# Kernel optimization log

Measured on AMD Instinct MI355X. Metric: run time of the kernel, lower is better.

Reference implementation:

```python
import jax, jax.numpy as jnp
import numpy as np

INPUT_DIM = 64
DIM = 256
N_EMB = 2048
M_BOOK = 4
MASK_RATIO = 0.1
N = 32768


def _bn(h, g, b):
    # BatchNorm1d in training mode: batch statistics (biased variance)
    mu = h.mean(axis=0)
    var = ((h - mu) ** 2).mean(axis=0)
    return (h - mu) * jax.lax.rsqrt(var + 1e-5) * g + b


def _quantize(r, E):
    # squared-distance via dot expansion: ||r||^2 - 2 r.E^T + ||E||^2  -> [N, K]
    d = (r * r).sum(axis=1, keepdims=True) - 2.0 * (r @ E.T) + (E * E).sum(axis=1)
    idx = jnp.argmin(d, axis=1)
    return E[idx]


def setup_inputs() -> dict:
    key = jax.random.key(0)
    ks = jax.random.split(key, 24)
    s = 0.02
    cb_lim = 1.0 / N_EMB
    inp = {
        "x": jax.random.normal(ks[0], (N, INPUT_DIM), jnp.float32),
        "pos": jax.random.uniform(ks[1], (1, INPUT_DIM), jnp.float32, -cb_lim, cb_lim),
        # encoder: Linear(64,128), BN128, Linear(128,256), BN256, Linear(256,256)
        "e_w0": jax.random.normal(ks[2], (INPUT_DIM, 128), jnp.float32) * s,
        "e_b0": jnp.zeros((128,), jnp.float32),
        "e_g0": jnp.ones((128,), jnp.float32),
        "e_bt0": jnp.zeros((128,), jnp.float32),
        "e_w1": jax.random.normal(ks[3], (128, 256), jnp.float32) * s,
        "e_b1": jnp.zeros((256,), jnp.float32),
        "e_g1": jnp.ones((256,), jnp.float32),
        "e_bt1": jnp.zeros((256,), jnp.float32),
        "e_w2": jax.random.normal(ks[4], (256, DIM), jnp.float32) * s,
        "e_b2": jnp.zeros((DIM,), jnp.float32),
        # codebooks: [M, K, C], uniform(-1/K, 1/K)
        "codebooks": jax.random.uniform(ks[5], (M_BOOK, N_EMB, DIM), jnp.float32, -cb_lim, cb_lim),
        # decoder: Linear(256,256), BN256, Linear(256,128), BN128, Linear(128,64)
        "d_w0": jax.random.normal(ks[6], (DIM, 256), jnp.float32) * s,
        "d_b0": jnp.zeros((256,), jnp.float32),
        "d_g0": jnp.ones((256,), jnp.float32),
        "d_bt0": jnp.zeros((256,), jnp.float32),
        "d_w1": jax.random.normal(ks[7], (256, 128), jnp.float32) * s,
        "d_b1": jnp.zeros((128,), jnp.float32),
        "d_g1": jnp.ones((128,), jnp.float32),
        "d_bt1": jnp.zeros((128,), jnp.float32),
        "d_w2": jax.random.normal(ks[8], (128, INPUT_DIM), jnp.float32) * s,
        "d_b2": jnp.zeros((INPUT_DIM,), jnp.float32),
    }
    return inp


def reference(x, pos, e_w0, e_b0, e_g0, e_bt0, e_w1, e_b1, e_g1, e_bt1, e_w2, e_b2,
              codebooks, d_w0, d_b0, d_g0, d_bt0, d_w1, d_b1, d_g1, d_bt1, d_w2, d_b2):
    # mask = x[0,:].bernoulli_(mask_ratio): in-place overwrites row 0 with 0/1 samples
    bern = jax.random.bernoulli(jax.random.key(42), MASK_RATIO, (x.shape[1],)).astype(x.dtype)
    x = x.at[0].set(bern)
    x = jnp.where(bern.astype(bool)[None, :], 0.0, x)
    x = x + pos

    # encoder (Dropout treated as identity / eval; BN uses batch stats as in training)
    h = jax.nn.relu(_bn(x @ e_w0 + e_b0, e_g0, e_bt0))
    h = jax.nn.relu(_bn(h @ e_w1 + e_b1, e_g1, e_bt1))
    ze = h @ e_w2 + e_b2  # [N, C]

    res_list, ce_list = [], []
    res = ze
    for m in range(M_BOOK):
        if m > 0:
            res = res_list[m - 1] - ce_list[m - 1]
        ce = _quantize(res, codebooks[m])
        res_list.append(res)
        ce_list.append(ce)

    zq = sum(ce_list)
    decoder_input = ze + jax.lax.stop_gradient(zq - ze)  # straight-through

    h = jax.nn.relu(_bn(decoder_input @ d_w0 + d_b0, d_g0, d_bt0))
    h = jax.nn.relu(_bn(h @ d_w1 + d_b1, d_g1, d_bt1))
    x_hat = h @ d_w2 + d_b2
    return x_hat, jnp.stack(res_list, 0), jnp.stack(ce_list, 0)
```

## Files before the change

kernel.cpp:

```cpp
#include <hip/hip_runtime.h>

#define N_ROWS 32768

typedef unsigned short u16;
typedef __attribute__((ext_vector_type(8))) short short8;
typedef __attribute__((ext_vector_type(4))) float f32x4;
typedef __attribute__((ext_vector_type(4))) u16 us4;

__device__ __forceinline__ unsigned rotl32(unsigned x, unsigned r) {
  return (x << r) | (x >> (32u - r));
}
__device__ __forceinline__ void tf_round(unsigned &x0, unsigned &x1, unsigned r) {
  x0 += x1; x1 = rotl32(x1, r); x1 ^= x0;
}

__global__ void mask_kernel(float* __restrict__ mask) {
  int j = threadIdx.x;
  if (j >= 64) return;
  const unsigned k0 = 0u, k1 = 42u;
  const unsigned k2 = 0x1BD11BDAu ^ k0 ^ k1;
  unsigned x0 = 0u;
  unsigned x1 = (unsigned)j;
  x0 += k0; x1 += k1;
  tf_round(x0, x1, 13); tf_round(x0, x1, 15); tf_round(x0, x1, 26); tf_round(x0, x1, 6);
  x0 += k1; x1 += k2 + 1u;
  tf_round(x0, x1, 17); tf_round(x0, x1, 29); tf_round(x0, x1, 16); tf_round(x0, x1, 24);
  x0 += k2; x1 += k0 + 2u;
  tf_round(x0, x1, 13); tf_round(x0, x1, 15); tf_round(x0, x1, 26); tf_round(x0, x1, 6);
  x0 += k0; x1 += k1 + 3u;
  tf_round(x0, x1, 17); tf_round(x0, x1, 29); tf_round(x0, x1, 16); tf_round(x0, x1, 24);
  x0 += k1; x1 += k2 + 4u;
  tf_round(x0, x1, 13); tf_round(x0, x1, 15); tf_round(x0, x1, 26); tf_round(x0, x1, 6);
  x0 += k2; x1 += k0 + 5u;
  unsigned bits = x0 ^ x1;
  float u = __uint_as_float((bits >> 9) | 0x3f800000u) - 1.0f;
  mask[j] = (u < 0.1f) ? 1.0f : 0.0f;
}

__global__ void norme_kernel(const float* __restrict__ cb, float* __restrict__ nE) {
#pragma clang fp contract(off)
  int k = blockIdx.x * blockDim.x + threadIdx.x;
  const float* r = cb + (size_t)k * 256;
  float halves[2];
#pragma unroll
  for (int h = 0; h < 2; h++) {
    float a[8];
#pragma unroll
    for (int j = 0; j < 8; j++) a[j] = 0.0f;
    for (int t = 0; t < 16; t++) {
      float4 v0 = *(const float4*)&r[h * 128 + 8 * t];
      float4 v1 = *(const float4*)&r[h * 128 + 8 * t + 4];
      a[0] = a[0] + v0.x * v0.x; a[1] = a[1] + v0.y * v0.y;
      a[2] = a[2] + v0.z * v0.z; a[3] = a[3] + v0.w * v0.w;
      a[4] = a[4] + v1.x * v1.x; a[5] = a[5] + v1.y * v1.y;
      a[6] = a[6] + v1.z * v1.z; a[7] = a[7] + v1.w * v1.w;
    }
    halves[h] = ((a[0] + a[1]) + (a[2] + a[3])) + ((a[4] + a[5]) + (a[6] + a[7]));
  }
  nE[k] = halves[0] + halves[1];
}

__global__ void rownorm_kernel(const float* __restrict__ R, float* __restrict__ rr) {
#pragma clang fp contract(off)
  int tid = threadIdx.x;
  int row = blockIdx.x * 64 + (tid >> 2);
  int q = tid & 3;
  int h = q >> 1;
  int j0 = (q & 1) << 2;
  const float* p = R + (size_t)row * 256 + h * 128 + j0;
  float a[4] = {0.f, 0.f, 0.f, 0.f};
  for (int t = 0; t < 16; t++) {
    float4 v = *(const float4*)&p[8 * t];
    a[0] = a[0] + v.x * v.x; a[1] = a[1] + v.y * v.y;
    a[2] = a[2] + v.z * v.z; a[3] = a[3] + v.w * v.w;
  }
  float s = (a[0] + a[1]) + (a[2] + a[3]);
  float half = s + __shfl_xor(s, 1, 4);
  float tot = half + __shfl_xor(half, 2, 4);
  if (q == 0) rr[row] = tot;
}

__device__ __forceinline__ u16 f2bf(float x) {
  unsigned u = __float_as_uint(x);
  unsigned r = u + 0x7fffu + ((u >> 16) & 1u);
  return (u16)(r >> 16);
}
__device__ __forceinline__ float bf2f(u16 h) {
  return __uint_as_float(((unsigned)h) << 16);
}

__global__ void cvt_kernel(const float* __restrict__ in, u16* __restrict__ out) {
  int gid = blockIdx.x * 256 + threadIdx.x;
  int row = gid >> 5, seg = gid & 31;
  const float* p = in + (size_t)row * 256 + seg * 8;
  u16* H = out + (size_t)row * 512 + seg * 8;
  float4 a = *(const float4*)p;
  float4 b = *(const float4*)(p + 4);
  float v[8] = {a.x, a.y, a.z, a.w, b.x, b.y, b.z, b.w};
  u16 hh[8], ll[8];
#pragma unroll
  for (int t = 0; t < 8; t++) {
    hh[t] = f2bf(v[t]);
    ll[t] = f2bf(v[t] - bf2f(hh[t]));
  }
  us4 H0 = {hh[0], hh[1], hh[2], hh[3]};
  us4 H1 = {hh[4], hh[5], hh[6], hh[7]};
  us4 L0 = {ll[0], ll[1], ll[2], ll[3]};
  us4 L1 = {ll[4], ll[5], ll[6], ll[7]};
  *(us4*)&H[0] = H0;  *(us4*)&H[4] = H1;
  *(us4*)&H[256] = L0; *(us4*)&H[260] = L1;
}

__global__ void bnprep_kernel(const double* __restrict__ psum, const double* __restrict__ psq,
                              const float* __restrict__ g, const float* __restrict__ bt,
                              float* __restrict__ a, float* __restrict__ c, int F) {
  int f = blockIdx.x * blockDim.x + threadIdx.x;
  if (f >= F) return;
  double s = 0.0, q = 0.0;
  const double* ps = psum + (size_t)f * 512;
  const double* pq = psq + (size_t)f * 512;
  for (int b = 0; b < 512; b++) { s += ps[b]; q += pq[b]; }
  double mu  = s * (1.0 / 32768.0);
  double var = q * (1.0 / 32768.0) - mu * mu;
  double inv = (double)g[f] / sqrt(var + 1e-5);
  a[f] = (float)inv;
  c[f] = (float)((double)bt[f] - mu * inv);
}

template <int MODE, int STATS>
__global__ __launch_bounds__(256)
void gemm64(const float* __restrict__ A, const float* __restrict__ W,
            const float* __restrict__ bias, const float* __restrict__ p0,
            const float* __restrict__ p1, const float* __restrict__ A3,
            float* __restrict__ out,
            double* __restrict__ psum, double* __restrict__ psq, int K, int F) {
  __shared__ float As[16][68];
  __shared__ float Bs[16][68];
  __shared__ double psumS[4][64];
  __shared__ double psqS[4][64];
  const int tid = threadIdx.x;
  const int row0 = blockIdx.y << 6;
  const int col0 = blockIdx.x << 6;
  const int ty = tid >> 4, tx = tid & 15;
  const int ar = tid >> 2, aq = (tid & 3) << 2;
  const int bk = tid >> 4, bc = (tid & 15) << 2;
  float acc[4][4] = {};
  for (int k0 = 0; k0 < K; k0 += 16) {
    const size_t aoff = (size_t)(row0 + ar) * K + k0 + aq;
    float4 av = *(const float4*)&A[aoff];
    float4 bv = *(const float4*)&W[(size_t)(k0 + bk) * F + col0 + bc];
    float a4[4] = { av.x, av.y, av.z, av.w };
    if (MODE == 0) {
#pragma unroll
      for (int j = 0; j < 4; j++) {
        int gk = k0 + aq + j;
        float m = p0[gk];
        float v = (m != 0.0f || (row0 + ar) == 0) ? 0.0f : a4[j];
        a4[j] = v + p1[gk];
      }
    } else if (MODE == 1) {
#pragma unroll
      for (int j = 0; j < 4; j++) {
        int gk = k0 + aq + j;
        a4[j] = fmaxf(fmaf(a4[j], p0[gk], p1[gk]), 0.0f);
      }
    } else if (MODE == 3) {
      float4 v1 = *(const float4*)&p0[aoff];
      float4 v2 = *(const float4*)&p1[aoff];
      float4 v3 = *(const float4*)&A3[aoff];
      a4[0] = ((a4[0] + v1.x) + v2.x) + v3.x;
      a4[1] = ((a4[1] + v1.y) + v2.y) + v3.y;
      a4[2] = ((a4[2] + v1.z) + v2.z) + v3.z;
      a4[3] = ((a4[3] + v1.w) + v2.w) + v3.w;
    }
    __syncthreads();
#pragma unroll
    for (int j = 0; j < 4; j++) As[aq + j][ar] = a4[j];
    *(float4*)&Bs[bk][bc] = bv;
    __syncthreads();
#pragma unroll
    for (int kc = 0; kc < 16; kc++) {
      float4 a = *(const float4*)&As[kc][ty << 2];
      float4 b = *(const float4*)&Bs[kc][tx << 2];
      float a_[4] = { a.x, a.y, a.z, a.w };
      float b_[4] = { b.x, b.y, b.z, b.w };
#pragma unroll
      for (int i = 0; i < 4; i++)
#pragma unroll
        for (int j = 0; j < 4; j++)
          acc[i][j] = fmaf(a_[i], b_[j], acc[i][j]);
    }
  }
  float bj[4];
#pragma unroll
  for (int j = 0; j < 4; j++) bj[j] = bias[col0 + (tx << 2) + j];
  double sj[4] = {}, qj[4] = {};
#pragma unroll
  for (int i = 0; i < 4; i++) {
    float v[4];
#pragma unroll
    for (int j = 0; j < 4; j++) {
      v[j] = acc[i][j] + bj[j];
      if (STATS) {
        sj[j] += (double)v[j];
        qj[j] += (double)v[j] * (double)v[j];
      }
    }
    float4 vv = { v[0], v[1], v[2], v[3] };
    *(float4*)&out[(size_t)(row0 + (ty << 2) + i) * F + col0 + (tx << 2)] = vv;
  }
  if (STATS) {
#pragma unroll
    for (int j = 0; j < 4; j++) {
      sj[j] += __shfl_down(sj[j], 32);
      sj[j] += __shfl_down(sj[j], 16);
      qj[j] += __shfl_down(qj[j], 32);
      qj[j] += __shfl_down(qj[j], 16);
    }
    const int w = tid >> 6;
    if ((tid & 63) < 16) {
#pragma unroll
      for (int j = 0; j < 4; j++) {
        psumS[w][((tid & 15) << 2) + j] = sj[j];
        psqS[w][((tid & 15) << 2) + j] = qj[j];
      }
    }
    __syncthreads();
    if (tid < 64) {
      double ds = (psumS[0][tid] + psumS[1][tid]) + (psumS[2][tid] + psumS[3][tid]);
      double dq = (psqS[0][tid] + psqS[1][tid]) + (psqS[2][tid] + psqS[3][tid]);
      psum[(size_t)(col0 + tid) * 512 + blockIdx.y] = ds;
      psq[(size_t)(col0 + tid) * 512 + blockIdx.y] = dq;
    }
  }
}

__device__ __forceinline__ void gld16(const void* gp, void* lp) {
  __builtin_amdgcn_global_load_lds(
      (__attribute__((address_space(1))) unsigned int*)gp,
      (__attribute__((address_space(3))) unsigned int*)lp,
      16, 0, 0);
}

#define MFMA16(a, b, c) __builtin_amdgcn_mfma_f32_16x16x32_bf16(a, b, c, 0, 0, 0)

__global__ __launch_bounds__(256, 2)
void quantize_mfma(const float* __restrict__ Rf, u16* Rcvt,
                   const float* __restrict__ Ef, const u16* __restrict__ Ecvt,
                   const float* __restrict__ nEp, const float* __restrict__ rr,
                   float* __restrict__ ce, float* __restrict__ resn) {
  __shared__ __align__(16) u16 As[2][64][32];
  __shared__ __align__(16) u16 Bs[2][128][32];
  __shared__ float sD1[2][64], sD2[2][64];
  __shared__ int sI1[2][64], sI2[2][64];
  __shared__ int s_iA[64], s_iB[64];

  const int tid = threadIdx.x;
  const int row0 = blockIdx.x << 6;
  const int w = tid >> 6;
  const int lane = tid & 63;
  const int wr = w >> 1, wc = w & 1;
  const int l15 = lane & 15, l4 = lane >> 4;

  float rrv[8];
#pragma unroll
  for (int s = 0; s < 8; s++)
    rrv[s] = rr[row0 + 32 * wr + 16 * (s >> 2) + 4 * l4 + (s & 3)];

  float bd1[8], bd2[8];
  int bi1[8], bi2[8];
#pragma unroll
  for (int s = 0; s < 8; s++) { bd1[s] = 3.0e38f; bd2[s] = 3.0e38f; bi1[s] = 0; bi2[s] = 1; }

  const int str = lane >> 2;
  const int sdst = (lane & 3) << 3;
  const int ssrc = (((lane & 3) ^ ((lane >> 3) & 3)) << 3);
  const int krd = ((l15 >> 1) & 3) << 3;

  for (int n0 = 0; n0 < 2048; n0 += 128) {
    f32x4 acc[2][4] = {};
    for (int k0 = 0; k0 < 256; k0 += 32) {
      __syncthreads();
      {
        const u16* gA = Rcvt + (size_t)(row0 + 16 * w + str) * 512 + k0 + ssrc;
        gld16(gA,       &As[0][16 * w + str][sdst]);
        gld16(gA + 256, &As[1][16 * w + str][sdst]);
#pragma unroll
        for (int q = 0; q < 2; q++) {
          const int rb = 32 * w + 16 * q + str;
          const u16* gB = Ecvt + (size_t)(n0 + rb) * 512 + k0 + ssrc;
          gld16(gB,       &Bs[0][rb][sdst]);
          gld16(gB + 256, &Bs[1][rb][sdst]);
        }
      }
      __syncthreads();
      short8 ah[2], al[2], bh[4], bl[4];
#pragma unroll
      for (int i = 0; i < 2; i++) {
        const int ro = 32 * wr + 16 * i + l15;
        ah[i] = *(const short8*)&As[0][ro][(l4 << 3) ^ krd];
        al[i] = *(const short8*)&As[1][ro][(l4 << 3) ^ krd];
      }
#pragma unroll
      for (int j = 0; j < 4; j++) {
        const int ro = 64 * wc + 16 * j + l15;
        bh[j] = *(const short8*)&Bs[0][ro][(l4 << 3) ^ krd];
        bl[j] = *(const short8*)&Bs[1][ro][(l4 << 3) ^ krd];
      }
#pragma unroll
      for (int i = 0; i < 2; i++)
#pragma unroll
        for (int j = 0; j < 4; j++) {
          acc[i][j] = MFMA16(ah[i], bh[j], acc[i][j]);
          acc[i][j] = MFMA16(ah[i], bl[j], acc[i][j]);
          acc[i][j] = MFMA16(al[i], bh[j], acc[i][j]);
        }
    }
#pragma unroll
    for (int j = 0; j < 4; j++) {
      const int col = n0 + 64 * wc + 16 * j + l15;
      const float nn = nEp[col];
#pragma unroll
      for (int i = 0; i < 2; i++)
#pragma unroll
        for (int r = 0; r < 4; r++) {
          const int s = i * 4 + r;
          float t = rrv[s] - 2.0f * acc[i][j][r];
          float d = t + nn;
          if (d < bd2[s]) {
            if (d < bd1[s]) {
              bd2[s] = bd1[s]; bi2[s] = bi1[s];
              bd1[s] = d; bi1[s] = col;
            } else {
              bd2[s] = d; bi2[s] = col;
            }
          }
        }
    }
  }

#pragma unroll
  for (int s = 0; s < 8; s++) {
    float d1 = bd1[s], d2 = bd2[s];
    int i1 = bi1[s], i2 = bi2[s];
#pragma unroll
    for (int off = 1; off <= 8; off <<= 1) {
      float e1 = __shfl_xor(d1, off, 16);
      float e2 = __shfl_xor(d2, off, 16);
      int j1 = __shfl_xor(i1, off, 16);
      int j2 = __shfl_xor(i2, off, 16);
      if (e1 < d1 || (e1 == d1 && j1 < i1)) {
        bool ps = (d1 < e2) || (d1 == e2 && i1 < j2);
        d2 = ps ? d1 : e2; i2 = ps ? i1 : j2;
        d1 = e1; i1 = j1;
      } else {
        bool ps = (e1 < d2) || (e1 == d2 && j1 < i2);
        if (ps) { d2 = e1; i2 = j1; }
      }
    }
    if (l15 == 0) {
      int lr = 32 * wr + 16 * (s >> 2) + 4 * l4 + (s & 3);
      sD1[wc][lr] = d1; sI1[wc][lr] = i1;
      sD2[wc][lr] = d2; sI2[wc][lr] = i2;
    }
  }
  __syncthreads();
  if (tid < 64) {
    float d1 = sD1[0][tid], d2 = sD2[0][tid];
    int i1 = sI1[0][tid], i2 = sI2[0][tid];
    float e1 = sD1[1][tid], e2 = sD2[1][tid];
    int j1 = sI1[1][tid], j2 = sI2[1][tid];
    int iA, iB;
    if (e1 < d1 || (e1 == d1 && j1 < i1)) {
      iA = j1;
      bool ps = (d1 < e2) || (d1 == e2 && i1 < j2);
      iB = ps ? i1 : j2;
    } else {
      iA = i1;
      bool ps = (e1 < d2) || (e1 == d2 && j1 < i2);
      iB = ps ? j1 : i2;
    }
    s_iA[tid] = iA; s_iB[tid] = iB;
  }
  __syncthreads();

  const int orow = tid >> 2;
  const int q = tid & 3;
  const int gr = row0 + orow;
  const int iA = s_iA[orow], iB = s_iB[orow];
  const float* __restrict__ Rr = Rf + (size_t)gr * 256;
  const float* __restrict__ EA = Ef + (size_t)iA * 256;
  const float* __restrict__ EB = Ef + (size_t)iB * 256;
  float pa[4] = {0.f, 0.f, 0.f, 0.f}, pb[4] = {0.f, 0.f, 0.f, 0.f};
  const int c0 = q << 6;
  for (int t = 0; t < 16; t++) {
    float4 rv = *(const float4*)&Rr[c0 + 4 * t];
    float4 ea = *(const float4*)&EA[c0 + 4 * t];
    float4 eb = *(const float4*)&EB[c0 + 4 * t];
    pa[0] = fmaf(rv.x, ea.x, pa[0]); pa[1] = fmaf(rv.y, ea.y, pa[1]);
    pa[2] = fmaf(rv.z, ea.z, pa[2]); pa[3] = fmaf(rv.w, ea.w, pa[3]);
    pb[0] = fmaf(rv.x, eb.x, pb[0]); pb[1] = fmaf(rv.y, eb.y, pb[1]);
    pb[2] = fmaf(rv.z, eb.z, pb[2]); pb[3] = fmaf(rv.w, eb.w, pb[3]);
  }
  float sA = (pa[0] + pa[1]) + (pa[2] + pa[3]);
  float sB = (pb[0] + pb[1]) + (pb[2] + pb[3]);
  sA += __shfl_xor(sA, 1, 4); sA += __shfl_xor(sA, 2, 4);
  sB += __shfl_xor(sB, 1, 4); sB += __shfl_xor(sB, 2, 4);
  const float rrow = rr[gr];
  float dA = (rrow - 2.0f * sA) + nEp[iA];
  float dB = (rrow - 2.0f * sB) + nEp[iB];
  const int idx = (dB < dA || (dB == dA && iB < iA)) ? iB : iA;

  const int oc0 = q << 6;
  const float* __restrict__ Er = Ef + (size_t)idx * 256;
  float* __restrict__ Cr = ce + (size_t)gr * 256;
  if (resn) {
    float* __restrict__ Nr = resn + (size_t)gr * 256;
    u16* Hr = Rcvt + (size_t)gr * 512;
    for (int c = oc0; c < oc0 + 64; c += 4) {
      float4 e = *(const float4*)&Er[c];
      float4 r = *(const float4*)&Rr[c];
      *(float4*)&Cr[c] = e;
      float4 dd = { r.x - e.x, r.y - e.y, r.z - e.z, r.w - e.w };
      *(float4*)&Nr[c] = dd;
      u16 h0 = f2bf(dd.x), h1 = f2bf(dd.y), h2 = f2bf(dd.z), h3 = f2bf(dd.w);
      us4 hv = { h0, h1, h2, h3 };
      us4 lv = { f2bf(dd.x - bf2f(h0)), f2bf(dd.y - bf2f(h1)),
                 f2bf(dd.z - bf2f(h2)), f2bf(dd.w - bf2f(h3)) };
      *(us4*)&Hr[c] = hv;
      *(us4*)&Hr[256 + c] = lv;
    }
  } else {
    for (int c = oc0; c < oc0 + 64; c += 4) {
      float4 e = *(const float4*)&Er[c];
      *(float4*)&Cr[c] = e;
    }
  }
}

extern "C" void kernel_launch(void* const* d_in, const int* in_sizes, int n_in,
                              void* d_out, int out_size, void* d_ws, size_t ws_size,
                              hipStream_t stream) {
  (void)in_sizes; (void)n_in; (void)out_size; (void)ws_size;
  const float* x     = (const float*)d_in[0];
  const float* pos   = (const float*)d_in[1];
  const float* e_w0  = (const float*)d_in[2];
  const float* e_b0  = (const float*)d_in[3];
  const float* e_g0  = (const float*)d_in[4];
  const float* e_bt0 = (const float*)d_in[5];
  const float* e_w1  = (const float*)d_in[6];
  const float* e_b1  = (const float*)d_in[7];
  const float* e_g1  = (const float*)d_in[8];
  const float* e_bt1 = (const float*)d_in[9];
  const float* e_w2  = (const float*)d_in[10];
  const float* e_b2  = (const float*)d_in[11];
  const float* cb    = (const float*)d_in[12];
  const float* d_w0  = (const float*)d_in[13];
  const float* d_b0  = (const float*)d_in[14];
  const float* d_g0  = (const float*)d_in[15];
  const float* d_bt0 = (const float*)d_in[16];
  const float* d_w1  = (const float*)d_in[17];
  const float* d_b1  = (const float*)d_in[18];
  const float* d_g1  = (const float*)d_in[19];
  const float* d_bt1 = (const float*)d_in[20];
  const float* d_w2  = (const float*)d_in[21];
  const float* d_b2  = (const float*)d_in[22];

  float* ws = (float*)d_ws;
  float* mask   = ws + 64;
  float* aff    = ws + 128;
  float* nE     = ws + 1664;
  double* psum  = (double*)(ws + 16384);
  double* psq   = (double*)(ws + 278528);
  float* g1     = ws + 540672;
  float* g0     = g1 + (size_t)N_ROWS * 256;
  float* rr     = g0 + (size_t)N_ROWS * 128;

  float* e0a = aff + 0;    float* e0c = aff + 128;
  float* e1a = aff + 256;  float* e1c = aff + 512;
  float* d0a = aff + 768;  float* d0c = aff + 1024;
  float* d1a = aff + 1280; float* d1c = aff + 1408;

  float* outp = (float*)d_out;
  float* xhat = outp;
  float* res0 = outp + (size_t)N_ROWS * 64;
  float* res1 = res0 + (size_t)N_ROWS * 256;
  float* res2 = res1 + (size_t)N_ROWS * 256;
  float* res3 = res2 + (size_t)N_ROWS * 256;
  float* ce0  = res0 + (size_t)4 * N_ROWS * 256;
  float* ce1  = ce0 + (size_t)N_ROWS * 256;
  float* ce2  = ce1 + (size_t)N_ROWS * 256;
  float* ce3  = ce2 + (size_t)N_ROWS * 256;

  float* h0 = ce2;
  float* h1 = ce3;
  u16* Ecvt = (u16*)xhat;
  u16* Rcvt = (u16*)ce3;

  mask_kernel<<<1, 64, 0, stream>>>(mask);
  norme_kernel<<<32, 256, 0, stream>>>(cb, nE);
  cvt_kernel<<<1024, 256, 0, stream>>>(cb, Ecvt);

  gemm64<0, 1><<<dim3(2, 512), 256, 0, stream>>>(x, e_w0, e_b0, mask, pos, nullptr,
                                                 h0, psum, psq, 64, 128);
  bnprep_kernel<<<1, 256, 0, stream>>>(psum, psq, e_g0, e_bt0, e0a, e0c, 128);
  gemm64<1, 1><<<dim3(4, 512), 256, 0, stream>>>(h0, e_w1, e_b1, e0a, e0c, nullptr,
                                                 h1, psum, psq, 128, 256);
  bnprep_kernel<<<1, 256, 0, stream>>>(psum, psq, e_g1, e_bt1, e1a, e1c, 256);
  gemm64<1, 0><<<dim3(4, 512), 256, 0, stream>>>(h1, e_w2, e_b2, e1a, e1c, nullptr,
                                                 res0, nullptr, nullptr, 256, 256);

  cvt_kernel<<<4096, 256, 0, stream>>>(res0, Rcvt);
  rownorm_kernel<<<512, 256, 0, stream>>>(res0, rr);
  quantize_mfma<<<512, 256, 0, stream>>>(res0, Rcvt,
                                         cb + (size_t)0 * 2048 * 256,
                                         Ecvt + (size_t)0 * 2048 * 512,
                                         nE + 0, rr, ce0, res1);
  rownorm_kernel<<<512, 256, 0, stream>>>(res1, rr);
  quantize_mfma<<<512, 256, 0, stream>>>(res1, Rcvt,
                                         cb + (size_t)1 * 2048 * 256,
                                         Ecvt + (size_t)1 * 2048 * 512,
                                         nE + 2048, rr, ce1, res2);
  rownorm_kernel<<<512, 256, 0, stream>>>(res2, rr);
  quantize_mfma<<<512, 256, 0, stream>>>(res2, Rcvt,
                                         cb + (size_t)2 * 2048 * 256,
                                         Ecvt + (size_t)2 * 2048 * 512,
                                         nE + 4096, rr, ce2, res3);
  rownorm_kernel<<<512, 256, 0, stream>>>(res3, rr);
  quantize_mfma<<<512, 256, 0, stream>>>(res3, Rcvt,
                                         cb + (size_t)3 * 2048 * 256,
                                         Ecvt + (size_t)3 * 2048 * 512,
                                         nE + 6144, rr, ce3, nullptr);

  gemm64<3, 1><<<dim3(4, 512), 256, 0, stream>>>(ce0, d_w0, d_b0, ce1, ce2, ce3,
                                                 g1, psum, psq, 256, 256);
  bnprep_kernel<<<1, 256, 0, stream>>>(psum, psq, d_g0, d_bt0, d0a, d0c, 256);
  gemm64<1, 1><<<dim3(2, 512), 256, 0, stream>>>(g1, d_w1, d_b1, d0a, d0c, nullptr,
                                                 g0, psum, psq, 256, 128);
  bnprep_kernel<<<1, 256, 0, stream>>>(psum, psq, d_g1, d_bt1, d1a, d1c, 128);
  gemm64<1, 0><<<dim3(1, 512), 256, 0, stream>>>(g0, d_w2, d_b2, d1a, d1c, nullptr,
                                                 xhat, nullptr, nullptr, 128, 64);
}
```

Before: 1.703 ms.

## Double-buffer LDS tiles in quantize kernel to overlap loads with MFMA

Flattens the nested codebook/K loops into a single 128-step loop and double-buffers the A and B LDS tiles. The next tile's global-to-LDS load is issued before computing on the current one, and only one barrier is needed per step. The codebook norm loads are also hoisted to the start of each column block. This doubles LDS use per block, which may limit occupancy at 2 blocks per CU, and the single barrier per step relies on the async LDS load being complete by the time that barrier is reached.

```diff
diff --git a/kernel.cpp b/kernel.cpp
--- a/kernel.cpp
+++ b/kernel.cpp
@@ -249,8 +249,8 @@
                    const float* __restrict__ Ef, const u16* __restrict__ Ecvt,
                    const float* __restrict__ nEp, const float* __restrict__ rr,
                    float* __restrict__ ce, float* __restrict__ resn) {
-  __shared__ __align__(16) u16 As[2][64][32];
-  __shared__ __align__(16) u16 Bs[2][128][32];
+  __shared__ __align__(16) u16 As[2][2][64][32];
+  __shared__ __align__(16) u16 Bs[2][2][128][32];
   __shared__ float sD1[2][64], sD2[2][64];
   __shared__ int sI1[2][64], sI2[2][64];
   __shared__ int s_iA[64], s_iB[64];
@@ -277,67 +277,93 @@
   const int ssrc = (((lane & 3) ^ ((lane >> 3) & 3)) << 3);
   const int krd = ((l15 >> 1) & 3) << 3;
 
-  for (int n0 = 0; n0 < 2048; n0 += 128) {
-    f32x4 acc[2][4] = {};
-    for (int k0 = 0; k0 < 256; k0 += 32) {
-      __syncthreads();
-      {
-        const u16* gA = Rcvt + (size_t)(row0 + 16 * w + str) * 512 + k0 + ssrc;
-        gld16(gA,       &As[0][16 * w + str][sdst]);
-        gld16(gA + 256, &As[1][16 * w + str][sdst]);
-#pragma unroll
-        for (int q = 0; q < 2; q++) {
-          const int rb = 32 * w + 16 * q + str;
-          const u16* gB = Ecvt + (size_t)(n0 + rb) * 512 + k0 + ssrc;
-          gld16(gB,       &Bs[0][rb][sdst]);
-          gld16(gB + 256, &Bs[1][rb][sdst]);
-        }
-      }
-      __syncthreads();
-      short8 ah[2], al[2], bh[4], bl[4];
-#pragma unroll
-      for (int i = 0; i < 2; i++) {
-        const int ro = 32 * wr + 16 * i + l15;
-        ah[i] = *(const short8*)&As[0][ro][(l4 << 3) ^ krd];
-        al[i] = *(const short8*)&As[1][ro][(l4 << 3) ^ krd];
-      }
+  const u16* gAbase = Rcvt + (size_t)(row0 + 16 * w + str) * 512 + ssrc;
+  const u16* gB0 = Ecvt + (size_t)(32 * w + str) * 512 + ssrc;
+  const u16* gB1 = Ecvt + (size_t)(32 * w + 16 + str) * 512 + ssrc;
+  const int rb0 = 32 * w + str, rb1 = 32 * w + 16 + str;
+
+#define STAGE(b, t)                                                         \
+  {                                                                         \
+    const int n0_ = ((t) >> 3) << 7, k0_ = ((t) & 7) << 5;                  \
+    const u16* gA_ = gAbase + k0_;                                          \
+    gld16(gA_,       &As[b][0][16 * w + str][sdst]);                        \
+    gld16(gA_ + 256, &As[b][1][16 * w + str][sdst]);                        \
+    const u16* g0_ = gB0 + (size_t)n0_ * 512 + k0_;                         \
+    const u16* g1_ = gB1 + (size_t)n0_ * 512 + k0_;                         \
+    gld16(g0_,       &Bs[b][0][rb0][sdst]);                                 \
+    gld16(g0_ + 256, &Bs[b][1][rb0][sdst]);                                 \
+    gld16(g1_,       &Bs[b][0][rb1][sdst]);                                 \
+    gld16(g1_ + 256, &Bs[b][1][rb1][sdst]);                                 \
+  }
+
+  STAGE(0, 0);
+  __syncthreads();
+
+  f32x4 acc[2][4] = {};
+  float nn4[4];
+#pragma unroll 2
+  for (int t = 0; t < 128; t++) {
+    const int b = t & 1;
+    if ((t & 7) == 0) {
+      const int n0 = (t >> 3) << 7;
+#pragma unroll
+      for (int j = 0; j < 4; j++) nn4[j] = nEp[n0 + 64 * wc + 16 * j + l15];
+    }
+    if (t + 1 < 128) STAGE(b ^ 1, t + 1);
+
+    short8 ah[2], al[2], bh[4], bl[4];
+#pragma unroll
+    for (int i = 0; i < 2; i++) {
+      const int ro = 32 * wr + 16 * i + l15;
+      ah[i] = *(const short8*)&As[b][0][ro][(l4 << 3) ^ krd];
+      al[i] = *(const short8*)&As[b][1][ro][(l4 << 3) ^ krd];
+    }
+#pragma unroll
+    for (int j = 0; j < 4; j++) {
+      const int ro = 64 * wc + 16 * j + l15;
+      bh[j] = *(const short8*)&Bs[b][0][ro][(l4 << 3) ^ krd];
+      bl[j] = *(const short8*)&Bs[b][1][ro][(l4 << 3) ^ krd];
+    }
+#pragma unroll
+    for (int i = 0; i < 2; i++)
 #pragma unroll
       for (int j = 0; j < 4; j++) {
-        const int ro = 64 * wc + 16 * j + l15;
-        bh[j] = *(const short8*)&Bs[0][ro][(l4 << 3) ^ krd];
-        bl[j] = *(const short8*)&Bs[1][ro][(l4 << 3) ^ krd];
-      }
-#pragma unroll
-      for (int i = 0; i < 2; i++)
-#pragma unroll
-        for (int j = 0; j < 4; j++) {
-          acc[i][j] = MFMA16(ah[i], bh[j], acc[i][j]);
-          acc[i][j] = MFMA16(ah[i], bl[j], acc[i][j]);
-          acc[i][j] = MFMA16(al[i], bh[j], acc[i][j]);
-        }
-    }
-#pragma unroll
-    for (int j = 0; j < 4; j++) {
-      const int col = n0 + 64 * wc + 16 * j + l15;
-      const float nn = nEp[col];
-#pragma unroll
-      for (int i = 0; i < 2; i++)
-#pragma unroll
-        for (int r = 0; r < 4; r++) {
-          const int s = i * 4 + r;
-          float t = rrv[s] - 2.0f * acc[i][j][r];
-          float d = t + nn;
-          if (d < bd2[s]) {
-            if (d < bd1[s]) {
-              bd2[s] = bd1[s]; bi2[s] = bi1[s];
-              bd1[s] = d; bi1[s] = col;
-            } else {
-              bd2[s] = d; bi2[s] = col;
+        acc[i][j] = MFMA16(ah[i], bh[j], acc[i][j]);
+        acc[i][j] = MFMA16(ah[i], bl[j], acc[i][j]);
+        acc[i][j] = MFMA16(al[i], bh[j], acc[i][j]);
+      }
+
+    if ((t & 7) == 7) {
+      const int n0 = (t >> 3) << 7;
+#pragma unroll
+      for (int j = 0; j < 4; j++) {
+        const int col = n0 + 64 * wc + 16 * j + l15;
+        const float nn = nn4[j];
+#pragma unroll
+        for (int i = 0; i < 2; i++)
+#pragma unroll
+          for (int r = 0; r < 4; r++) {
+            const int s = i * 4 + r;
+            float tt = rrv[s] - 2.0f * acc[i][j][r];
+            float d = tt + nn;
+            if (d < bd2[s]) {
+              if (d < bd1[s]) {
+                bd2[s] = bd1[s]; bi2[s] = bi1[s];
+                bd1[s] = d; bi1[s] = col;
+              } else {
+                bd2[s] = d; bi2[s] = col;
+              }
             }
           }
-        }
-    }
-  }
+      }
+#pragma unroll
+      for (int i = 0; i < 2; i++)
+#pragma unroll
+        for (int j = 0; j < 4; j++) acc[i][j] = f32x4{0.f, 0.f, 0.f, 0.f};
+    }
+    __syncthreads();
+  }
+#undef STAGE
 
 #pragma unroll
   for (int s = 0; s < 8; s++) {
```

Result: faster. 1.650 ms (-3.1%).
